# Performance work log

Hardware: AMD Instinct MI355X
Metric: run time of the kernel (lower is better)

## Reference

```python
import jax, jax.numpy as jnp
import numpy as np
from jax import lax

# PyTorch LSTM cell: gate order i, f, g, o; bias_ih + bias_hh folded into one b.
def _cell(carry, x, Wih, Whh, b):
    h, c = carry
    g = x @ Wih.T + h @ Whh.T + b
    i, f, gg, o = jnp.split(g, 4, axis=-1)
    c = jax.nn.sigmoid(f) * c + jax.nn.sigmoid(i) * jnp.tanh(gg)
    h = jax.nn.sigmoid(o) * jnp.tanh(c)
    return (h, c), h

def _bidir_layer(x_seq, Wih, Whh, b):
    # x_seq: [S, B, D]; Wih: [2, 4H, D] (dir 0 = fwd, 1 = bwd)
    B = x_seq.shape[1]
    H = Whh.shape[-1]
    z0 = (jnp.zeros((B, H), x_seq.dtype), jnp.zeros((B, H), x_seq.dtype))
    (hf, cf), of = lax.scan(lambda ca, x: _cell(ca, x, Wih[0], Whh[0], b[0]), z0, x_seq)
    (hb, cb), ob = lax.scan(lambda ca, x: _cell(ca, x, Wih[1], Whh[1], b[1]), z0, x_seq[::-1])
    out = jnp.concatenate([of, ob[::-1]], axis=-1)  # [S, B, 2H], time-aligned
    return out, (hf, cf), (hb, cb)


def setup_inputs() -> dict:
    key = jax.random.key(0)
    ks = jax.random.split(key, 26)
    V, E, H, S, B, T = 50000, 300, 512, 400, 32, 15
    def rn(k, shape, s=0.05):
        return (jax.random.normal(k, shape, jnp.float32) * s)
    return {
        "article": jax.random.randint(ks[0], (S, B), 0, V),
        "summary": jax.random.randint(ks[1], (T, B), 0, V),
        "z_noise": jax.random.normal(ks[2], (B, H), jnp.float32),
        "enc_emb": rn(ks[3], (V, E), 0.1),
        "enc_l0_Wih": rn(ks[4], (2, 4 * H, E)),
        "enc_l0_Whh": rn(ks[5], (2, 4 * H, H)),
        "enc_l0_b": rn(ks[6], (2, 4 * H)),
        "enc_l1_Wih": rn(ks[7], (2, 4 * H, 2 * H)),
        "enc_l1_Whh": rn(ks[8], (2, 4 * H, H)),
        "enc_l1_b": rn(ks[9], (2, 4 * H)),
        "mu_W": rn(ks[10], (H, H)),
        "mu_b": rn(ks[11], (H,)),
        "lv_W": rn(ks[12], (H, H)),
        "lv_b": rn(ks[13], (H,)),
        "dec_hid_W": rn(ks[14], (H, H)),
        "dec_hid_b": rn(ks[15], (H,)),
        "dec_emb": rn(ks[16], (V, E), 0.1),
        "dec_l0_Wih": rn(ks[17], (2, 4 * H, E)),
        "dec_l0_Whh": rn(ks[18], (2, 4 * H, H)),
        "dec_l0_b": rn(ks[19], (2, 4 * H)),
        "dec_l1_Wih": rn(ks[20], (2, 4 * H, 2 * H)),
        "dec_l1_Whh": rn(ks[21], (2, 4 * H, H)),
        "dec_l1_b": rn(ks[22], (2, 4 * H)),
        "pred_W": rn(ks[23], (V, 2 * H)),
        "pred_b": rn(ks[24], (V,)),
    }


def reference(article, summary, z_noise, enc_emb,
              enc_l0_Wih, enc_l0_Whh, enc_l0_b,
              enc_l1_Wih, enc_l1_Whh, enc_l1_b,
              mu_W, mu_b, lv_W, lv_b,
              dec_hid_W, dec_hid_b, dec_emb,
              dec_l0_Wih, dec_l0_Whh, dec_l0_b,
              dec_l1_Wih, dec_l1_Whh, dec_l1_b,
              pred_W, pred_b):
    # ---- encoder: embedding + 2-layer bidirectional LSTM ----
    emb = enc_emb[article]  # [S, B, E]
    o0, (h0f, c0f), (h0b, c0b) = _bidir_layer(emb, enc_l0_Wih, enc_l0_Whh, enc_l0_b)
    o1, (h1f, c1f), (h1b, c1b) = _bidir_layer(o0, enc_l1_Wih, enc_l1_Whh, enc_l1_b)
    hid = jnp.stack([h0f, h0b, h1f, h1b])   # [4, B, H] (torch layout l0f,l0b,l1f,l1b)
    c_enc = jnp.stack([c0f, c0b, c1f, c1b])

    # ---- VAE reparameterization ----
    mu = hid @ mu_W.T + mu_b            # [4, B, H]
    logvar = hid @ lv_W.T + lv_b
    z = z_noise * jnp.exp(0.5 * logvar) + mu  # broadcast [B,H] -> [4,B,H]

    # ---- decoder: greedy argmax feedback loop (self.tf is None) ----
    h_init = z @ dec_hid_W.T + dec_hid_b  # [4, B, H]

    def step(carry, _):
        dec_in, h, c = carry
        x = dec_emb[dec_in]  # [B, E]
        (h0f_, c0f_), _o = _cell((h[0], c[0]), x, dec_l0_Wih[0], dec_l0_Whh[0], dec_l0_b[0])
        (h0b_, c0b_), _o = _cell((h[1], c[1]), x, dec_l0_Wih[1], dec_l0_Whh[1], dec_l0_b[1])
        x1 = jnp.concatenate([h0f_, h0b_], axis=-1)  # [B, 2H]
        (h1f_, c1f_), _o = _cell((h[2], c[2]), x1, dec_l1_Wih[0], dec_l1_Whh[0], dec_l1_b[0])
        (h1b_, c1b_), _o = _cell((h[3], c[3]), x1, dec_l1_Wih[1], dec_l1_Whh[1], dec_l1_b[1])
        out = jnp.concatenate([h1f_, h1b_], axis=-1)  # [B, 2H]
        p = jax.nn.log_softmax(out @ pred_W.T + pred_b, axis=1)  # [B, V]
        h_new = jnp.stack([h0f_, h0b_, h1f_, h1b_])
        c_new = jnp.stack([c0f_, c0b_, c1f_, c1b_])
        return (jnp.argmax(p, axis=1), h_new, c_new), p

    T = summary.shape[0]
    _, outs = lax.scan(step, (summary[0], h_init, c_enc), None, length=T)  # [T, B, V]
    return (outs, mu, logvar, z)
```

## Files before the change

kernel.cpp:

```cpp
#include <hip/hip_runtime.h>
#include <math.h>

typedef _Float16 f16;
typedef __attribute__((__ext_vector_type__(8))) _Float16 f16x8;
typedef __attribute__((__ext_vector_type__(4))) float f32x4;
typedef __attribute__((__ext_vector_type__(2))) float fv2;

static __device__ __forceinline__ f32x4 mfma16(f16x8 a, f16x8 b, f32x4 c) {
  return __builtin_amdgcn_mfma_f32_16x16x32_f16(a, b, c, 0, 0, 0);
}
static __device__ __forceinline__ float sigf(float x) { return 1.0f / (1.0f + expf(-x)); }
static __device__ __forceinline__ void split2(float v, f16* hi, f16* lo) {
  f16 h = (f16)v;
  *hi = h;
  *lo = (f16)((v - (float)h) * 2048.0f);
}
static __device__ __forceinline__ unsigned packh(f16 a, f16 b) {
  union { f16 f; unsigned short u; } ua, ub;
  ua.f = a; ub.f = b;
  return (unsigned)ua.u | ((unsigned)ub.u << 16);
}
union H4 { f16 f[4]; uint2 u; };

struct Seg {
  const float* src; const int* idx; f16* hi; f16* lo;
  long end;
  int cs, cd;
};
struct SegTab { Seg s[13]; };

__global__ void k_prep(SegTab tab, long total, unsigned* bar) {
  if (blockIdx.x == 0 && threadIdx.x < 256) {
    bar[threadIdx.x] = 0;
    bar[threadIdx.x + 256] = 0;
  }
  for (long pos = (long)blockIdx.x * 256 + threadIdx.x; pos < total;
       pos += (long)gridDim.x * 256) {
    long start = 0; int si = 0;
    while (pos >= tab.s[si].end) { start = tab.s[si].end; ++si; }
    const Seg g = tab.s[si];
    long local = pos - start;
    float v;
    if (g.cd == 320) {
      unsigned l32 = (unsigned)local;
      unsigned r = l32 / 320u, c = l32 - r * 320u;
      long row = g.idx ? (long)g.idx[r] : (long)r;
      v = (c < 300u) ? g.src[row * 300 + c] : 0.0f;
    } else {
      v = g.src[local];
    }
    split2(v, &g.hi[local], &g.lo[local]);
  }
}

template <int BM>
__global__ __launch_bounds__(256, 1) void k_gemm(
    const f16* __restrict__ Ahi, const f16* __restrict__ Alo,
    const f16* __restrict__ Bhi, const f16* __restrict__ Blo,
    const float* __restrict__ bias, float* __restrict__ C,
    int M, int N, int K, long aB, long bB, long cB) {
  constexpr int MF = (BM == 128) ? 4 : 2;
  constexpr int NF = (BM == 128) ? 4 : 2;
  constexpr int ACH = BM * 8 / 256;
  __shared__ f16 sA[2][BM][72];
  __shared__ f16 sB[2][128][72];

  const int tid = threadIdx.x;
  const int wid = tid >> 6, lane = tid & 63;
  const int ln = lane & 15, l4 = lane >> 4;
  const int m0 = blockIdx.y * BM;
  const int n0 = blockIdx.x * 128;
  const int z = blockIdx.z;
  const f16* pA[2] = {Ahi + (long)z * aB, Alo + (long)z * aB};
  const f16* pB[2] = {Bhi + (long)z * bB, Blo + (long)z * bB};
  float* pC = C + (long)z * cB;

  const int wrow = (BM == 128) ? (wid >> 1) * 64 : 0;
  const int wcol = (BM == 128) ? (wid & 1) * 64 : wid * 32;

  f32x4 am[MF][NF], ax[MF][NF];
#pragma unroll
  for (int i = 0; i < MF; ++i)
#pragma unroll
    for (int j = 0; j < NF; ++j) {
      am[i][j] = (f32x4){0.f, 0.f, 0.f, 0.f};
      ax[i][j] = (f32x4){0.f, 0.f, 0.f, 0.f};
    }

  uint4 ra[2][ACH], rb[2][4];
  auto load_regs = [&](int k0) {
#pragma unroll
    for (int p = 0; p < 2; ++p) {
#pragma unroll
      for (int q = 0; q < ACH; ++q) {
        const int i = tid + q * 256;
        const int r = i >> 3, ch = i & 7;
        const int gr = m0 + r;
        uint4 v = make_uint4(0u, 0u, 0u, 0u);
        if (gr < M) v = *(const uint4*)(pA[p] + (long)gr * K + k0 + ch * 8);
        ra[p][q] = v;
      }
#pragma unroll
      for (int q = 0; q < 4; ++q) {
        const int i = tid + q * 256;
        const int r = i >> 3, ch = i & 7;
        const int gn = n0 + r;
        uint4 v = make_uint4(0u, 0u, 0u, 0u);
        if (gn < N) v = *(const uint4*)(pB[p] + (long)gn * K + k0 + ch * 8);
        rb[p][q] = v;
      }
    }
  };

  load_regs(0);
  for (int k0 = 0; k0 < K; k0 += 64) {
    __syncthreads();
#pragma unroll
    for (int p = 0; p < 2; ++p) {
#pragma unroll
      for (int q = 0; q < ACH; ++q) {
        const int i = tid + q * 256;
        *(uint4*)&sA[p][i >> 3][(i & 7) * 8] = ra[p][q];
      }
#pragma unroll
      for (int q = 0; q < 4; ++q) {
        const int i = tid + q * 256;
        *(uint4*)&sB[p][i >> 3][(i & 7) * 8] = rb[p][q];
      }
    }
    __syncthreads();
    if (k0 + 64 < K) load_regs(k0 + 64);
#pragma unroll
    for (int kk = 0; kk < 64; kk += 32) {
      const int kc = kk + l4 * 8;
      f16x8 ah[MF], al[MF], bh[NF], bl[NF];
#pragma unroll
      for (int i = 0; i < MF; ++i) {
        ah[i] = *(const f16x8*)&sA[0][wrow + i * 16 + ln][kc];
        al[i] = *(const f16x8*)&sA[1][wrow + i * 16 + ln][kc];
      }
#pragma unroll
      for (int j = 0; j < NF; ++j) {
        bh[j] = *(const f16x8*)&sB[0][wcol + j * 16 + ln][kc];
        bl[j] = *(const f16x8*)&sB[1][wcol + j * 16 + ln][kc];
      }
#pragma unroll
      for (int i = 0; i < MF; ++i)
#pragma unroll
        for (int j = 0; j < NF; ++j) {
          am[i][j] = mfma16(ah[i], bh[j], am[i][j]);
          ax[i][j] = mfma16(ah[i], bl[j], ax[i][j]);
          ax[i][j] = mfma16(al[i], bh[j], ax[i][j]);
        }
    }
  }
#pragma unroll
  for (int i = 0; i < MF; ++i)
#pragma unroll
    for (int j = 0; j < NF; ++j) {
      int row = m0 + wrow + i * 16 + l4 * 4;
      int col = n0 + wcol + j * 16 + ln;
      if (col < N) {
        float bv = bias ? bias[col] : 0.0f;
#pragma unroll
        for (int r = 0; r < 4; ++r)
          if (row + r < M)
            pC[(long)(row + r) * N + col] = am[i][j][r] + ax[i][j][r] * (1.0f / 2048.0f) + bv;
      }
    }
}

__global__ __launch_bounds__(256, 1) void k_lstm(
    const f16* __restrict__ WhhHi, const f16* __restrict__ WhhLo,
    const float* __restrict__ Gx,
    f16* __restrict__ hHi, f16* __restrict__ hLo,
    f16* __restrict__ oHi, f16* __restrict__ oLo,
    float* __restrict__ hidOut, f16* __restrict__ hidOutH, f16* __restrict__ hidOutL,
    float* __restrict__ cOut,
    unsigned* __restrict__ bar, int S, int layer) {
  const int tid = threadIdx.x;
  const int d = blockIdx.x >> 5;
  const int wg = blockIdx.x & 31;
  const int j0 = wg * 16;

  __shared__ f16 sHh[32][520];
  __shared__ f16 sHl[32][520];
  __shared__ float sGate[2][4][32][16];

  const int wid = tid >> 6, lane = tid & 63;
  const int gh = wid & 1, kh = wid >> 1;
  const int ln = lane & 15, lk8 = (lane >> 4) * 8;

  f16x8 wbh[2][8], wbl[2][8];
#pragma unroll
  for (int gl = 0; gl < 2; ++gl) {
    const long rowb = ((long)d * 2048 + (gh * 2 + gl) * 512 + j0 + ln) << 9;
#pragma unroll
    for (int ks = 0; ks < 8; ++ks) {
      const long off = rowb + (kh * 8 + ks) * 32 + lk8;
      wbh[gl][ks] = *(const f16x8*)(WhhHi + off);
      wbl[gl][ks] = *(const f16x8*)(WhhLo + off);
    }
  }

  unsigned* flags = bar + d * 64;
  const unsigned* myFlag = flags + (tid & 31);
  const int cb = tid >> 3;
  const int cj = (tid & 7) * 2;
  float creg0 = 0.0f, creg1 = 0.0f;

  {
    long zo = ((long)d * 32 + cb) * 512 + j0 + cj;
    unsigned zero = 0;
    char* zh = (char*)(hHi + zo);
    char* zl = (char*)(hLo + zo);
    asm volatile("global_store_dword %0, %1, off sc0 sc1" ::"v"(zh), "v"(zero) : "memory");
    asm volatile("global_store_dword %0, %1, off sc0 sc1" ::"v"(zl), "v"(zero) : "memory");
    asm volatile("s_waitcnt vmcnt(0) lgkmcnt(0)" ::: "memory");
    __builtin_amdgcn_s_barrier();
    if (tid == 0) {
      unsigned one = 1u;
      asm volatile("global_store_dword %0, %1, off sc0 sc1" ::"v"(flags + wg), "v"(one)
                   : "memory");
    }
    for (;;) {
      unsigned v;
      asm volatile("global_load_dword %0, %1, off sc0 sc1" : "=v"(v) : "v"(myFlag) : "memory");
      asm volatile("s_waitcnt vmcnt(0)" ::: "memory");
      if (__all(v >= 1u)) break;
      __builtin_amdgcn_s_sleep(1);
    }
    __builtin_amdgcn_sched_barrier(0);
  }

  for (int t = 0; t < S; ++t) {
    const int trow = d ? (S - 1 - t) : t;
    const int par = t & 1;

    uint4 hv[16];
    {
      const char* hb = (const char*)(hHi + ((long)par * 2 + d) * 32 * 512);
      const char* lb = (const char*)(hLo + ((long)par * 2 + d) * 32 * 512);
#pragma unroll
      for (int q = 0; q < 8; ++q) {
        const char* p = hb + (((long)q * 256 + tid) << 4);
        asm volatile("global_load_dwordx4 %0, %1, off sc0 sc1" : "=v"(hv[q]) : "v"(p));
      }
#pragma unroll
      for (int q = 0; q < 8; ++q) {
        const char* p = lb + (((long)q * 256 + tid) << 4);
        asm volatile("global_load_dwordx4 %0, %1, off sc0 sc1" : "=v"(hv[8 + q]) : "v"(p));
      }
    }
    fv2 gxv[4];
#pragma unroll
    for (int g = 0; g < 4; ++g) {
      const char* p = (const char*)&Gx[((long)trow * 32 + cb) * 4096 + (long)d * 2048 +
                                       g * 512 + j0 + cj];
      asm volatile("global_load_dwordx2 %0, %1, off" : "=v"(gxv[g]) : "v"(p));
    }
    asm volatile("s_waitcnt vmcnt(4)" ::: "memory");
    __builtin_amdgcn_sched_barrier(0);
#pragma unroll
    for (int q = 0; q < 8; ++q) {
      int c = q * 256 + tid;
      *(uint4*)&sHh[c >> 6][(c & 63) * 8] = hv[q];
      *(uint4*)&sHl[c >> 6][(c & 63) * 8] = hv[8 + q];
    }
    asm volatile("s_waitcnt lgkmcnt(0)" ::: "memory");
    __builtin_amdgcn_s_barrier();

    f32x4 am[2][2], ax[2][2];
#pragma unroll
    for (int a = 0; a < 2; ++a)
#pragma unroll
      for (int b2 = 0; b2 < 2; ++b2) {
        am[a][b2] = (f32x4){0.f, 0.f, 0.f, 0.f};
        ax[a][b2] = (f32x4){0.f, 0.f, 0.f, 0.f};
      }
#pragma unroll
    for (int ks = 0; ks < 8; ++ks) {
      const int kc = (kh * 8 + ks) * 32 + lk8;
      f16x8 a0h = *(const f16x8*)&sHh[ln][kc];
      f16x8 a1h = *(const f16x8*)&sHh[16 + ln][kc];
      f16x8 a0l = *(const f16x8*)&sHl[ln][kc];
      f16x8 a1l = *(const f16x8*)&sHl[16 + ln][kc];
#pragma unroll
      for (int gl = 0; gl < 2; ++gl) {
        am[gl][0] = mfma16(a0h, wbh[gl][ks], am[gl][0]);
        ax[gl][0] = mfma16(a0h, wbl[gl][ks], ax[gl][0]);
        ax[gl][0] = mfma16(a0l, wbh[gl][ks], ax[gl][0]);
        am[gl][1] = mfma16(a1h, wbh[gl][ks], am[gl][1]);
        ax[gl][1] = mfma16(a1h, wbl[gl][ks], ax[gl][1]);
        ax[gl][1] = mfma16(a1l, wbh[gl][ks], ax[gl][1]);
      }
    }

#pragma unroll
    for (int gl = 0; gl < 2; ++gl) {
      const int g = gh * 2 + gl;
#pragma unroll
      for (int mf = 0; mf < 2; ++mf) {
        const int row = mf * 16 + (lane >> 4) * 4;
#pragma unroll
        for (int r = 0; r < 4; ++r)
          sGate[kh][g][row + r][ln] = am[gl][mf][r] + ax[gl][mf][r] * (1.0f / 2048.0f);
      }
    }
    asm volatile("s_waitcnt lgkmcnt(0)" ::: "memory");
    __builtin_amdgcn_s_barrier();

    asm volatile("s_waitcnt vmcnt(0)" ::: "memory");
    __builtin_amdgcn_sched_barrier(0);

    {
      float i0 = sGate[0][0][cb][cj] + sGate[1][0][cb][cj] + gxv[0][0];
      float i1 = sGate[0][0][cb][cj + 1] + sGate[1][0][cb][cj + 1] + gxv[0][1];
      float f0 = sGate[0][1][cb][cj] + sGate[1][1][cb][cj] + gxv[1][0];
      float f1 = sGate[0][1][cb][cj + 1] + sGate[1][1][cb][cj + 1] + gxv[1][1];
      float g0 = sGate[0][2][cb][cj] + sGate[1][2][cb][cj] + gxv[2][0];
      float g1 = sGate[0][2][cb][cj + 1] + sGate[1][2][cb][cj + 1] + gxv[2][1];
      float o0 = sGate[0][3][cb][cj] + sGate[1][3][cb][cj] + gxv[3][0];
      float o1 = sGate[0][3][cb][cj + 1] + sGate[1][3][cb][cj + 1] + gxv[3][1];
      float c0 = sigf(f0) * creg0 + sigf(i0) * tanhf(g0);
      float c1 = sigf(f1) * creg1 + sigf(i1) * tanhf(g1);
      creg0 = c0; creg1 = c1;
      float h0 = sigf(o0) * tanhf(c0);
      float h1 = sigf(o1) * tanhf(c1);
      f16 h0h, h0l, h1h, h1l;
      split2(h0, &h0h, &h0l);
      split2(h1, &h1h, &h1l);
      unsigned phi = packh(h0h, h1h), plo = packh(h0l, h1l);
      long ho = ((((long)(par ^ 1) * 2 + d) * 32 + cb) * 512 + j0 + cj);
      char* dh = (char*)(hHi + ho);
      char* dl = (char*)(hLo + ho);
      asm volatile("global_store_dword %0, %1, off sc0 sc1" ::"v"(dh), "v"(phi) : "memory");
      asm volatile("global_store_dword %0, %1, off sc0 sc1" ::"v"(dl), "v"(plo) : "memory");
      if (oHi) {
        long oo = ((long)trow * 32 + cb) * 1024 + (long)d * 512 + j0 + cj;
        *(unsigned*)(oHi + oo) = phi;
        *(unsigned*)(oLo + oo) = plo;
      }
      if (t == S - 1) {
        long so = (((long)layer * 2 + d) * 32 + cb) * 512 + j0 + cj;
        *(float2*)(hidOut + so) = make_float2(h0, h1);
        *(unsigned*)(hidOutH + so) = phi;
        *(unsigned*)(hidOutL + so) = plo;
        *(float2*)(cOut + so) = make_float2(c0, c1);
      }
    }

    asm volatile("s_waitcnt vmcnt(0) lgkmcnt(0)" ::: "memory");
    __builtin_amdgcn_s_barrier();
    const unsigned tg = (unsigned)t + 2u;
    if (tid == 0) {
      asm volatile("global_store_dword %0, %1, off sc0 sc1" ::"v"(flags + wg), "v"(tg)
                   : "memory");
    }
    for (;;) {
      unsigned v;
      asm volatile("global_load_dword %0, %1, off sc0 sc1" : "=v"(v) : "v"(myFlag) : "memory");
      asm volatile("s_waitcnt vmcnt(0)" ::: "memory");
      if (__all(v >= tg)) break;
      __builtin_amdgcn_s_sleep(1);
    }
    __builtin_amdgcn_sched_barrier(0);
  }
}

template <int XK, bool GATHER>
static __device__ __forceinline__ void dec_body(
    int sub, const int* __restrict__ tok, const float* __restrict__ emb,
    const f16* __restrict__ xH, const f16* __restrict__ xL,
    const f16* __restrict__ WihH, const f16* __restrict__ WihL,
    const f16* __restrict__ WhhH, const f16* __restrict__ WhhL,
    const float* __restrict__ bias,
    const f16* __restrict__ dhInH, const f16* __restrict__ dhInL,
    f16* __restrict__ dhOutH, f16* __restrict__ dhOutL,
    float* __restrict__ cDec, f16* __restrict__ xoH, f16* __restrict__ xoL,
    int layer, f16 (&sA)[2][32][72], f16 (&sB)[2][64][72], float (&sGate)[4][32][17]) {
  const int tid = threadIdx.x;
  const int d = sub >> 5;
  const int jt = sub & 31;
  const int s = layer * 2 + d;

  const int wid = tid >> 6, lane = tid & 63;
  const int ln = lane & 15, l4 = lane >> 4;
  const int ar = tid >> 3, ach = tid & 7;
  constexpr int NK = XK / 64 + 8;

  int tk = 0;
  if (GATHER) tk = tok[ar];

  f32x4 am[2], ax[2];
#pragma unroll
  for (int i = 0; i < 2; ++i) {
    am[i] = (f32x4){0.f, 0.f, 0.f, 0.f};
    ax[i] = (f32x4){0.f, 0.f, 0.f, 0.f};
  }

  uint4 ra0, ra1, rb[4];
  float gaf[8];

  auto load_regs = [&](int k) {
    const int k0 = k * 64;
    if (k0 < XK) {
      if (GATHER) {
        const float* rowp = emb + (long)tk * 300;
        const int c4 = k0 + ach * 8;
#pragma unroll
        for (int h = 0; h < 2; ++h) {
          float4 v = make_float4(0.f, 0.f, 0.f, 0.f);
          if (c4 + h * 4 < 300) v = *(const float4*)(rowp + c4 + h * 4);
          gaf[h * 4 + 0] = v.x; gaf[h * 4 + 1] = v.y;
          gaf[h * 4 + 2] = v.z; gaf[h * 4 + 3] = v.w;
        }
      } else {
        ra0 = *(const uint4*)(xH + (long)ar * XK + k0 + ach * 8);
        ra1 = *(const uint4*)(xL + (long)ar * XK + k0 + ach * 8);
      }
    } else {
      const int hk = k0 - XK;
      ra0 = *(const uint4*)(dhInH + ((long)s * 32 + ar) * 512 + hk + ach * 8);
      ra1 = *(const uint4*)(dhInL + ((long)s * 32 + ar) * 512 + hk + ach * 8);
    }
#pragma unroll
    for (int q = 0; q < 2; ++q) {
      const int i = tid + q * 256;
      const int r = i >> 3, ch = i & 7;
      const long srow = (long)d * 2048 + (r >> 4) * 512 + jt * 16 + (r & 15);
      if (k0 < XK) {
        rb[q * 2] = *(const uint4*)(WihH + srow * XK + k0 + ch * 8);
        rb[q * 2 + 1] = *(const uint4*)(WihL + srow * XK + k0 + ch * 8);
      } else {
        const int hk = k0 - XK;
        rb[q * 2] = *(const uint4*)(WhhH + srow * 512 + hk + ch * 8);
        rb[q * 2 + 1] = *(const uint4*)(WhhL + srow * 512 + hk + ch * 8);
      }
    }
  };

  load_regs(0);
  for (int k = 0; k < NK; ++k) {
    const bool gw = GATHER && (k * 64 < XK);
    __syncthreads();
    if (gw) {
#pragma unroll
      for (int u = 0; u < 8; ++u)
        split2(gaf[u], &sA[0][ar][ach * 8 + u], &sA[1][ar][ach * 8 + u]);
    } else {
      *(uint4*)&sA[0][ar][ach * 8] = ra0;
      *(uint4*)&sA[1][ar][ach * 8] = ra1;
    }
#pragma unroll
    for (int q = 0; q < 2; ++q) {
      const int i = tid + q * 256;
      const int r = i >> 3, ch = i & 7;
      *(uint4*)&sB[0][r][ch * 8] = rb[q * 2];
      *(uint4*)&sB[1][r][ch * 8] = rb[q * 2 + 1];
    }
    __syncthreads();
    if (k + 1 < NK) load_regs(k + 1);
#pragma unroll
    for (int kk = 0; kk < 64; kk += 32) {
      const int kc = kk + l4 * 8;
      f16x8 a0h = *(const f16x8*)&sA[0][ln][kc];
      f16x8 a1h = *(const f16x8*)&sA[0][16 + ln][kc];
      f16x8 a0l = *(const f16x8*)&sA[1][ln][kc];
      f16x8 a1l = *(const f16x8*)&sA[1][16 + ln][kc];
      f16x8 bh = *(const f16x8*)&sB[0][wid * 16 + ln][kc];
      f16x8 bl = *(const f16x8*)&sB[1][wid * 16 + ln][kc];
      am[0] = mfma16(a0h, bh, am[0]);
      ax[0] = mfma16(a0h, bl, ax[0]);
      ax[0] = mfma16(a0l, bh, ax[0]);
      am[1] = mfma16(a1h, bh, am[1]);
      ax[1] = mfma16(a1h, bl, ax[1]);
      ax[1] = mfma16(a1l, bh, ax[1]);
    }
  }

#pragma unroll
  for (int i2 = 0; i2 < 2; ++i2)
#pragma unroll
    for (int r = 0; r < 4; ++r)
      sGate[wid][i2 * 16 + l4 * 4 + r][ln] = am[i2][r] + ax[i2][r] * (1.0f / 2048.0f);
  __syncthreads();

  {
    const int b = tid >> 3, cj = (tid & 7) * 2;
    const int j = jt * 16 + cj;
    float iv0 = sGate[0][b][cj] + bias[d * 2048 + j];
    float iv1 = sGate[0][b][cj + 1] + bias[d * 2048 + j + 1];
    float fv0 = sGate[1][b][cj] + bias[d * 2048 + 512 + j];
    float fv1 = sGate[1][b][cj + 1] + bias[d * 2048 + 512 + j + 1];
    float gv0 = sGate[2][b][cj] + bias[d * 2048 + 1024 + j];
    float gv1 = sGate[2][b][cj + 1] + bias[d * 2048 + 1024 + j + 1];
    float ov0 = sGate[3][b][cj] + bias[d * 2048 + 1536 + j];
    float ov1 = sGate[3][b][cj + 1] + bias[d * 2048 + 1536 + j + 1];
    long co = ((long)s * 32 + b) * 512 + j;
    float2 cold = *(const float2*)&cDec[co];
    float c0 = sigf(fv0) * cold.x + sigf(iv0) * tanhf(gv0);
    float c1 = sigf(fv1) * cold.y + sigf(iv1) * tanhf(gv1);
    *(float2*)&cDec[co] = make_float2(c0, c1);
    float h0 = sigf(ov0) * tanhf(c0);
    float h1 = sigf(ov1) * tanhf(c1);
    f16 h0h, h0l, h1h, h1l;
    split2(h0, &h0h, &h0l);
    split2(h1, &h1h, &h1l);
    unsigned phi = packh(h0h, h1h), plo = packh(h0l, h1l);
    *(unsigned*)&dhOutH[co] = phi;
    *(unsigned*)&dhOutL[co] = plo;
    long xo = (long)b * 1024 + d * 512 + j;
    *(unsigned*)&xoH[xo] = phi;
    *(unsigned*)&xoL[xo] = plo;
  }
}

template <int XK, bool GATHER>
__global__ __launch_bounds__(256, 1) void k_dec(
    const int* __restrict__ tok, const float* __restrict__ emb,
    const f16* __restrict__ xH, const f16* __restrict__ xL,
    const f16* __restrict__ WihH, const f16* __restrict__ WihL,
    const f16* __restrict__ WhhH, const f16* __restrict__ WhhL,
    const float* __restrict__ bias,
    const f16* __restrict__ dhInH, const f16* __restrict__ dhInL,
    f16* __restrict__ dhOutH, f16* __restrict__ dhOutL,
    float* __restrict__ cDec, f16* __restrict__ xoH, f16* __restrict__ xoL,
    int layer) {
  __shared__ f16 sA[2][32][72];
  __shared__ f16 sB[2][64][72];
  __shared__ float sGate[4][32][17];
  dec_body<XK, GATHER>(blockIdx.x, tok, emb, xH, xL, WihH, WihL, WhhH, WhhL, bias,
                       dhInH, dhInL, dhOutH, dhOutL, cDec, xoH, xoL, layer, sA, sB,
                       sGate);
}

__global__ __launch_bounds__(256, 1) void k_pred(
    const f16* __restrict__ xH, const f16* __restrict__ xL,
    const f16* __restrict__ BH, const f16* __restrict__ BL,
    const float* __restrict__ bias, float* __restrict__ C) {
  __shared__ f16 sAh[32][1032];
  __shared__ f16 sAl[32][1032];
  const int tid = threadIdx.x;
#pragma unroll
  for (int q = 0; q < 16; ++q) {
    int idx = tid + q * 256;
    int r = idx >> 7, c8 = idx & 127;
    *(uint4*)&sAh[r][c8 * 8] = *(const uint4*)(xH + r * 1024 + c8 * 8);
    *(uint4*)&sAl[r][c8 * 8] = *(const uint4*)(xL + r * 1024 + c8 * 8);
  }
  __syncthreads();

  const int wid = tid >> 6, lane = tid & 63;
  const int ln = lane & 15, l4 = lane >> 4;
  const int n0 = blockIdx.x * 128 + wid * 32;

  const int row0 = n0 + ln, row1 = n0 + 16 + ln;
  const f16* pbh0 = BH + (long)(row0 < 50000 ? row0 : 0) * 1024 + l4 * 8;
  const f16* pbl0 = BL + (long)(row0 < 50000 ? row0 : 0) * 1024 + l4 * 8;
  const f16* pbh1 = BH + (long)(row1 < 50000 ? row1 : 0) * 1024 + l4 * 8;
  const f16* pbl1 = BL + (long)(row1 < 50000 ? row1 : 0) * 1024 + l4 * 8;

  f32x4 am[2][2], ax[2][2];
#pragma unroll
  for (int i = 0; i < 2; ++i)
#pragma unroll
    for (int j = 0; j < 2; ++j) {
      am[i][j] = (f32x4){0.f, 0.f, 0.f, 0.f};
      ax[i][j] = (f32x4){0.f, 0.f, 0.f, 0.f};
    }

  f16x8 b0[4], b1[4], b2[4], b3[4];
  auto loadB = [&](int s, f16x8* buf) {
    const long o = (long)s * 32;
    buf[0] = *(const f16x8*)(pbh0 + o);
    buf[1] = *(const f16x8*)(pbl0 + o);
    buf[2] = *(const f16x8*)(pbh1 + o);
    buf[3] = *(const f16x8*)(pbl1 + o);
  };
  auto comp = [&](int s, const f16x8* buf) {
    const int kc = s * 32 + l4 * 8;
    f16x8 a0h = *(const f16x8*)&sAh[ln][kc];
    f16x8 a1h = *(const f16x8*)&sAh[16 + ln][kc];
    f16x8 a0l = *(const f16x8*)&sAl[ln][kc];
    f16x8 a1l = *(const f16x8*)&sAl[16 + ln][kc];
    am[0][0] = mfma16(a0h, buf[0], am[0][0]);
    ax[0][0] = mfma16(a0h, buf[1], ax[0][0]);
    ax[0][0] = mfma16(a0l, buf[0], ax[0][0]);
    am[1][0] = mfma16(a1h, buf[0], am[1][0]);
    ax[1][0] = mfma16(a1h, buf[1], ax[1][0]);
    ax[1][0] = mfma16(a1l, buf[0], ax[1][0]);
    am[0][1] = mfma16(a0h, buf[2], am[0][1]);
    ax[0][1] = mfma16(a0h, buf[3], ax[0][1]);
    ax[0][1] = mfma16(a0l, buf[2], ax[0][1]);
    am[1][1] = mfma16(a1h, buf[2], am[1][1]);
    ax[1][1] = mfma16(a1h, buf[3], ax[1][1]);
    ax[1][1] = mfma16(a1l, buf[2], ax[1][1]);
  };

  loadB(0, b0);
  loadB(1, b1);
  loadB(2, b2);
#pragma unroll 1
  for (int s = 0; s < 32; s += 4) {
    loadB(s + 3, b3);
    comp(s, b0);
    loadB(s + 4, b0);
    comp(s + 1, b1);
    loadB(s + 5, b1);
    comp(s + 2, b2);
    loadB(s + 6, b2);
    comp(s + 3, b3);
  }

#pragma unroll
  for (int j = 0; j < 2; ++j) {
    const int col = n0 + j * 16 + ln;
    if (col < 50000) {
      const float bv = bias[col];
#pragma unroll
      for (int i = 0; i < 2; ++i)
#pragma unroll
        for (int r = 0; r < 4; ++r) {
          const int row = i * 16 + l4 * 4 + r;
          C[(long)row * 50000 + col] = am[i][j][r] + ax[i][j][r] * (1.0f / 2048.0f) + bv;
        }
    }
  }
}

__global__ void k_vae(const float* __restrict__ mlOut, const float* __restrict__ mub,
                      const float* __restrict__ lvb, const float* __restrict__ zn,
                      float* __restrict__ outMu, float* __restrict__ outLv,
                      float* __restrict__ outZ, f16* __restrict__ zHi,
                      f16* __restrict__ zLo) {
  int i = blockIdx.x * 256 + threadIdx.x;
  if (i >= 4 * 32 * 512) return;
  int bj = i & (32 * 512 - 1);
  int j = i & 511;
  float m = mlOut[i] + mub[j];
  float l = mlOut[65536 + i] + lvb[j];
  float z = zn[bj] * expf(0.5f * l) + m;
  outMu[i] = m;
  outLv[i] = l;
  outZ[i] = z;
  split2(z, &zHi[i], &zLo[i]);
}

__global__ void k_decinit(const float* __restrict__ hInit, const float* __restrict__ cEnc,
                          const int* __restrict__ summary, f16* __restrict__ dhHi,
                          f16* __restrict__ dhLo, float* __restrict__ cDec,
                          int* __restrict__ tok) {
  int i = blockIdx.x * 256 + threadIdx.x;
  if (i < 4 * 32 * 512) {
    split2(hInit[i], &dhHi[i], &dhLo[i]);
    cDec[i] = cEnc[i];
  }
  if (i < 32) tok[i] = summary[i];
}

__global__ __launch_bounds__(256) void k_lsm(const float* __restrict__ logits,
                                             float* __restrict__ outs,
                                             int* __restrict__ tok, int t) {
  const int b = blockIdx.x;
  const int tid = threadIdx.x;
  const float* lg = logits + (long)b * 50000;
  float m = -INFINITY, s = 0.0f;
  int am = 0;
  for (int v = tid; v < 50000; v += 256) {
    float x = lg[v];
    if (x > m) {
      s = s * expf(m - x) + 1.0f;
      m = x;
      am = v;
    } else {
      s += expf(x - m);
    }
  }
  __shared__ float sm[256], ss[256];
  __shared__ int sa[256];
  sm[tid] = m; ss[tid] = s; sa[tid] = am;
  __syncthreads();
  for (int o = 128; o > 0; o >>= 1) {
    if (tid < o) {
      float m2 = sm[tid + o], s2 = ss[tid + o];
      int a2 = sa[tid + o];
      float m1 = sm[tid], s1 = ss[tid];
      int a1 = sa[tid];
      if (m2 > m1 || (m2 == m1 && a2 < a1)) {
        sm[tid] = m2; ss[tid] = s2 + s1 * expf(m1 - m2); sa[tid] = a2;
      } else {
        ss[tid] = s1 + s2 * expf(m2 - m1);
      }
    }
    __syncthreads();
  }
  float lse = sm[0] + logf(ss[0]);
  float* ob = outs + ((long)t * 32 + b) * 50000;
  for (int v = tid; v < 50000; v += 256) ob[v] = lg[v] - lse;
  if (tid == 0) tok[b] = sa[0];
}

extern "C" void kernel_launch(void* const* d_in, const int* in_sizes, int n_in,
                              void* d_out, int out_size, void* d_ws, size_t ws_size,
                              hipStream_t stream) {
  const int* article = (const int*)d_in[0];
  const int* summary = (const int*)d_in[1];
  const float* z_noise = (const float*)d_in[2];
  const float* enc_emb = (const float*)d_in[3];
  const float* e0Wih = (const float*)d_in[4];
  const float* e0Whh = (const float*)d_in[5];
  const float* e0b = (const float*)d_in[6];
  const float* e1Wih = (const float*)d_in[7];
  const float* e1Whh = (const float*)d_in[8];
  const float* e1b = (const float*)d_in[9];
  const float* muW = (const float*)d_in[10];
  const float* mub = (const float*)d_in[11];
  const float* lvW = (const float*)d_in[12];
  const float* lvb = (const float*)d_in[13];
  const float* dhW = (const float*)d_in[14];
  const float* dhb = (const float*)d_in[15];
  const float* dec_emb = (const float*)d_in[16];
  const float* d0Wih = (const float*)d_in[17];
  const float* d0Whh = (const float*)d_in[18];
  const float* d0b = (const float*)d_in[19];
  const float* d1Wih = (const float*)d_in[20];
  const float* d1Whh = (const float*)d_in[21];
  const float* d1b = (const float*)d_in[22];
  const float* predW = (const float*)d_in[23];
  const float* predb = (const float*)d_in[24];
  float* out = (float*)d_out;
  (void)in_sizes; (void)n_in; (void)out_size; (void)ws_size;

  char* w = (char*)d_ws;
  size_t off = 0;
  auto alloc = [&](size_t bytes) -> void* {
    void* p = w + off;
    off += (bytes + 255) & ~(size_t)255;
    return p;
  };

  f16* e0WihH = (f16*)alloc(4096L * 320 * 2);
  f16* e0WihL = (f16*)alloc(4096L * 320 * 2);
  f16* e0WhhH = (f16*)alloc(4096L * 512 * 2);
  f16* e0WhhL = (f16*)alloc(4096L * 512 * 2);
  f16* e1WihH = (f16*)alloc(4096L * 1024 * 2);
  f16* e1WihL = (f16*)alloc(4096L * 1024 * 2);
  f16* e1WhhH = (f16*)alloc(4096L * 512 * 2);
  f16* e1WhhL = (f16*)alloc(4096L * 512 * 2);
  f16* d0WihH = (f16*)alloc(4096L * 320 * 2);
  f16* d0WihL = (f16*)alloc(4096L * 320 * 2);
  f16* d0WhhH = (f16*)alloc(4096L * 512 * 2);
  f16* d0WhhL = (f16*)alloc(4096L * 512 * 2);
  f16* d1WihH = (f16*)alloc(4096L * 1024 * 2);
  f16* d1WihL = (f16*)alloc(4096L * 1024 * 2);
  f16* d1WhhH = (f16*)alloc(4096L * 512 * 2);
  f16* d1WhhL = (f16*)alloc(4096L * 512 * 2);
  f16* mlWH = (f16*)alloc(2L * 262144 * 2);
  f16* mlWL = (f16*)alloc(2L * 262144 * 2);
  f16* dhWH = (f16*)alloc(512L * 512 * 2);
  f16* dhWL = (f16*)alloc(512L * 512 * 2);
  f16* predH = (f16*)alloc(50000L * 1024 * 2);
  f16* predL = (f16*)alloc(50000L * 1024 * 2);
  f16* embH = (f16*)alloc(12800L * 320 * 2);
  f16* embL = (f16*)alloc(12800L * 320 * 2);
  f16* o0H = (f16*)alloc(12800L * 1024 * 2);
  f16* o0L = (f16*)alloc(12800L * 1024 * 2);
  float* Gx = (float*)alloc(12800L * 4096 * 4);
  f16* hEncH = (f16*)alloc(2L * 2 * 32 * 512 * 2);
  f16* hEncL = (f16*)alloc(2L * 2 * 32 * 512 * 2);
  float* hid = (float*)alloc(128L * 512 * 4);
  float* cEnc = (float*)alloc(128L * 512 * 4);
  f16* hidH = (f16*)alloc(128L * 512 * 2);
  f16* hidL = (f16*)alloc(128L * 512 * 2);
  float* mlOut = (float*)alloc(2L * 65536 * 4);
  f16* zH = (f16*)alloc(128L * 512 * 2);
  f16* zL = (f16*)alloc(128L * 512 * 2);
  float* hInit = (float*)alloc(128L * 512 * 4);
  f16* dhH = (f16*)alloc(2L * 65536 * 2);
  f16* dhL = (f16*)alloc(2L * 65536 * 2);
  float* cDec = (float*)alloc(4L * 32 * 512 * 4);
  f16* x1H = (f16*)alloc(32L * 1024 * 2);
  f16* x1L = (f16*)alloc(32L * 1024 * 2);
  f16* x2H = (f16*)alloc(32L * 1024 * 2);
  f16* x2L = (f16*)alloc(32L * 1024 * 2);
  float* logits = (float*)alloc(32L * 50000 * 4);
  int* tok = (int*)alloc(256);
  unsigned* bar = (unsigned*)alloc(2048);

  SegTab tab;
  long cum = 0;
  int si = 0;
  auto seg = [&](const float* src, const int* idx, f16* hi, f16* lo, long rows, int cs,
                 int cd) {
    cum += rows * cd;
    tab.s[si++] = Seg{src, idx, hi, lo, cum, cs, cd};
  };
  seg(e0Wih, nullptr, e0WihH, e0WihL, 4096, 300, 320);
  seg(e0Whh, nullptr, e0WhhH, e0WhhL, 4096, 512, 512);
  seg(e1Wih, nullptr, e1WihH, e1WihL, 4096, 1024, 1024);
  seg(e1Whh, nullptr, e1WhhH, e1WhhL, 4096, 512, 512);
  seg(d0Wih, nullptr, d0WihH, d0WihL, 4096, 300, 320);
  seg(d0Whh, nullptr, d0WhhH, d0WhhL, 4096, 512, 512);
  seg(d1Wih, nullptr, d1WihH, d1WihL, 4096, 1024, 1024);
  seg(d1Whh, nullptr, d1WhhH, d1WhhL, 4096, 512, 512);
  seg(muW, nullptr, mlWH, mlWL, 512, 512, 512);
  seg(lvW, nullptr, mlWH + 262144, mlWL + 262144, 512, 512, 512);
  seg(dhW, nullptr, dhWH, dhWL, 512, 512, 512);
  seg(predW, nullptr, predH, predL, 50000, 1024, 1024);
  seg(enc_emb, article, embH, embL, 12800, 300, 320);
  k_prep<<<8192, 256, 0, stream>>>(tab, cum, bar);

  k_gemm<128><<<dim3(32, 100, 1), 256, 0, stream>>>(embH, embL, e0WihH, e0WihL, e0b, Gx,
                                                    12800, 4096, 320, 0, 0, 0);
  k_lstm<<<64, 256, 0, stream>>>(e0WhhH, e0WhhL, Gx, hEncH, hEncL, o0H, o0L, hid, hidH,
                                 hidL, cEnc, bar, 400, 0);
  k_gemm<128><<<dim3(32, 100, 1), 256, 0, stream>>>(o0H, o0L, e1WihH, e1WihL, e1b, Gx,
                                                    12800, 4096, 1024, 0, 0, 0);
  k_lstm<<<64, 256, 0, stream>>>(e1WhhH, e1WhhL, Gx, hEncH, hEncL, (f16*)nullptr,
                                 (f16*)nullptr, hid, hidH, hidL, cEnc, bar + 128, 400, 1);

  k_gemm<32><<<dim3(4, 4, 2), 256, 0, stream>>>(hidH, hidL, mlWH, mlWL,
                                                (const float*)nullptr, mlOut, 128, 512,
                                                512, 0, 262144, 65536);
  k_vae<<<256, 256, 0, stream>>>(mlOut, mub, lvb, z_noise, out + 24000000L,
                                 out + 24065536L, out + 24131072L, zH, zL);
  k_gemm<32><<<dim3(4, 4, 1), 256, 0, stream>>>(zH, zL, dhWH, dhWL, dhb, hInit, 128, 512,
                                                512, 0, 0, 0);
  k_decinit<<<256, 256, 0, stream>>>(hInit, cEnc, summary, dhH, dhL, cDec, tok);

  for (int t = 0; t < 15; ++t) {
    int par = t & 1;
    f16* dIH = dhH + (long)par * 65536;
    f16* dIL = dhL + (long)par * 65536;
    f16* dOH = dhH + (long)(par ^ 1) * 65536;
    f16* dOL = dhL + (long)(par ^ 1) * 65536;
    k_dec<320, true><<<64, 256, 0, stream>>>(tok, dec_emb, (const f16*)nullptr,
                                             (const f16*)nullptr, d0WihH, d0WihL, d0WhhH,
                                             d0WhhL, d0b, dIH, dIL, dOH, dOL, cDec, x1H,
                                             x1L, 0);
    k_dec<1024, false><<<64, 256, 0, stream>>>((const int*)nullptr, (const float*)nullptr,
                                               x1H, x1L, d1WihH, d1WihL, d1WhhH, d1WhhL,
                                               d1b, dIH, dIL, dOH, dOL, cDec, x2H, x2L,
                                               1);
    k_pred<<<391, 256, 0, stream>>>(x2H, x2L, predH, predL, predb, logits);
    k_lsm<<<32, 256, 0, stream>>>(logits, out, tok, t);
  }
}
```

Before: 7.487 ms.

## Spin on grid barrier with one wave and halve k_pred LDS for two blocks per CU

New measurement: 7.557 ms. About the same (+0.9%).

```diff
diff --git a/kernel.cpp b/kernel.cpp
--- a/kernel.cpp
+++ b/kernel.cpp
@@ -204,7 +204,7 @@
   }
 
   unsigned* flags = bar + d * 64;
-  const unsigned* myFlag = flags + (tid & 31);
+  const unsigned* myFlag = flags + (lane & 31);
   const int cb = tid >> 3;
   const int cj = (tid & 7) * 2;
   float creg0 = 0.0f, creg1 = 0.0f;
@@ -218,18 +218,21 @@
     asm volatile("global_store_dword %0, %1, off sc0 sc1" ::"v"(zl), "v"(zero) : "memory");
     asm volatile("s_waitcnt vmcnt(0) lgkmcnt(0)" ::: "memory");
     __builtin_amdgcn_s_barrier();
-    if (tid == 0) {
-      unsigned one = 1u;
-      asm volatile("global_store_dword %0, %1, off sc0 sc1" ::"v"(flags + wg), "v"(one)
-                   : "memory");
-    }
-    for (;;) {
-      unsigned v;
-      asm volatile("global_load_dword %0, %1, off sc0 sc1" : "=v"(v) : "v"(myFlag) : "memory");
-      asm volatile("s_waitcnt vmcnt(0)" ::: "memory");
-      if (__all(v >= 1u)) break;
-      __builtin_amdgcn_s_sleep(1);
-    }
+    if (wid == 0) {
+      if (lane == 0) {
+        unsigned one = 1u;
+        asm volatile("global_store_dword %0, %1, off sc0 sc1" ::"v"(flags + wg), "v"(one)
+                     : "memory");
+      }
+      for (;;) {
+        unsigned v;
+        asm volatile("global_load_dword %0, %1, off sc0 sc1" : "=v"(v) : "v"(myFlag) : "memory");
+        asm volatile("s_waitcnt vmcnt(0)" ::: "memory");
+        if (__all(v >= 1u)) break;
+        __builtin_amdgcn_s_sleep(1);
+      }
+    }
+    __builtin_amdgcn_s_barrier();
     __builtin_amdgcn_sched_barrier(0);
   }
 
@@ -353,17 +356,20 @@
     asm volatile("s_waitcnt vmcnt(0) lgkmcnt(0)" ::: "memory");
     __builtin_amdgcn_s_barrier();
     const unsigned tg = (unsigned)t + 2u;
-    if (tid == 0) {
-      asm volatile("global_store_dword %0, %1, off sc0 sc1" ::"v"(flags + wg), "v"(tg)
-                   : "memory");
-    }
-    for (;;) {
-      unsigned v;
-      asm volatile("global_load_dword %0, %1, off sc0 sc1" : "=v"(v) : "v"(myFlag) : "memory");
-      asm volatile("s_waitcnt vmcnt(0)" ::: "memory");
-      if (__all(v >= tg)) break;
-      __builtin_amdgcn_s_sleep(1);
-    }
+    if (wid == 0) {
+      if (lane == 0) {
+        asm volatile("global_store_dword %0, %1, off sc0 sc1" ::"v"(flags + wg), "v"(tg)
+                     : "memory");
+      }
+      for (;;) {
+        unsigned v;
+        asm volatile("global_load_dword %0, %1, off sc0 sc1" : "=v"(v) : "v"(myFlag) : "memory");
+        asm volatile("s_waitcnt vmcnt(0)" ::: "memory");
+        if (__all(v >= tg)) break;
+        __builtin_amdgcn_s_sleep(1);
+      }
+    }
+    __builtin_amdgcn_s_barrier();
     __builtin_amdgcn_sched_barrier(0);
   }
 }
@@ -535,21 +541,23 @@
                        sGate);
 }
 
-__global__ __launch_bounds__(256, 1) void k_pred(
+__global__ __launch_bounds__(256, 2) void k_pred(
     const f16* __restrict__ xH, const f16* __restrict__ xL,
     const f16* __restrict__ BH, const f16* __restrict__ BL,
     const float* __restrict__ bias, float* __restrict__ C) {
-  __shared__ f16 sAh[32][1032];
-  __shared__ f16 sAl[32][1032];
+  __shared__ f16 sAh[32][520];
+  __shared__ f16 sAl[32][520];
   const int tid = threadIdx.x;
-#pragma unroll
-  for (int q = 0; q < 16; ++q) {
-    int idx = tid + q * 256;
-    int r = idx >> 7, c8 = idx & 127;
-    *(uint4*)&sAh[r][c8 * 8] = *(const uint4*)(xH + r * 1024 + c8 * 8);
-    *(uint4*)&sAl[r][c8 * 8] = *(const uint4*)(xL + r * 1024 + c8 * 8);
-  }
-  __syncthreads();
+
+  auto stageA = [&](int koff) {
+#pragma unroll
+    for (int q = 0; q < 8; ++q) {
+      int idx = tid + q * 256;
+      int r = idx >> 6, c8 = idx & 63;
+      *(uint4*)&sAh[r][c8 * 8] = *(const uint4*)(xH + r * 1024 + koff + c8 * 8);
+      *(uint4*)&sAl[r][c8 * 8] = *(const uint4*)(xL + r * 1024 + koff + c8 * 8);
+    }
+  };
 
   const int wid = tid >> 6, lane = tid & 63;
   const int ln = lane & 15, l4 = lane >> 4;
@@ -579,7 +587,7 @@
     buf[3] = *(const f16x8*)(pbl1 + o);
   };
   auto comp = [&](int s, const f16x8* buf) {
-    const int kc = s * 32 + l4 * 8;
+    const int kc = (s & 15) * 32 + l4 * 8;
     f16x8 a0h = *(const f16x8*)&sAh[ln][kc];
     f16x8 a1h = *(const f16x8*)&sAh[16 + ln][kc];
     f16x8 a0l = *(const f16x8*)&sAl[ln][kc];
@@ -598,19 +606,29 @@
     ax[1][1] = mfma16(a1l, buf[2], ax[1][1]);
   };
 
+  stageA(0);
   loadB(0, b0);
   loadB(1, b1);
   loadB(2, b2);
+  __syncthreads();
+#pragma unroll
+  for (int h = 0; h < 2; ++h) {
+    if (h) {
+      __syncthreads();
+      stageA(512);
+      __syncthreads();
+    }
 #pragma unroll 1
-  for (int s = 0; s < 32; s += 4) {
-    loadB(s + 3, b3);
-    comp(s, b0);
-    loadB(s + 4, b0);
-    comp(s + 1, b1);
-    loadB(s + 5, b1);
-    comp(s + 2, b2);
-    loadB(s + 6, b2);
-    comp(s + 3, b3);
+    for (int s = h * 16; s < h * 16 + 16; s += 4) {
+      loadB(s + 3, b3);
+      comp(s, b0);
+      loadB(s + 4, b0);
+      comp(s + 1, b1);
+      loadB(s + 5, b1);
+      comp(s + 2, b2);
+      loadB(s + 6, b2);
+      comp(s + 3, b3);
+    }
   }
 
 #pragma unroll
```
